# Optimization experiments

Hardware: AMD Instinct MI355X
Metric: run time of the kernel (lower is better)

## Reference

```python
import jax, jax.numpy as jnp
import numpy as np

B, IN, H = 4096, 1024, 1024

def setup_inputs() -> dict:
    key = jax.random.key(0)
    ks = jax.random.split(key, 8)
    s = 1.0 / np.sqrt(IN + H)  # ~torch Linear init scale
    return {
        "x": jax.random.normal(ks[0], (B, IN), jnp.float32),
        "h_prev": jax.random.normal(ks[1], (B, H), jnp.float32),
        "c_prev": jax.random.normal(ks[2], (B, H), jnp.float32),
        "Wf": jax.random.normal(ks[3], (IN + H, H), jnp.float32) * s,
        "bf": jnp.zeros((H,), jnp.float32),
        "Wi": jax.random.normal(ks[4], (IN + H, H), jnp.float32) * s,
        "bi": jnp.zeros((H,), jnp.float32),
        "Wg": jax.random.normal(ks[5], (IN + H, H), jnp.float32) * s,
        "bg": jnp.zeros((H,), jnp.float32),
        "Wo": jax.random.normal(ks[6], (IN + H, H), jnp.float32) * s,
        "bo": jnp.zeros((H,), jnp.float32),
    }

def reference(x, h_prev, c_prev, Wf, bf, Wi, bi, Wg, bg, Wo, bo):
    combined = jnp.concatenate([x, h_prev], axis=1)          # [B, IN+H]
    # fuse the 4 gate projections into one GEMM: [B, IN+H] x [IN+H, 4H]
    W = jnp.concatenate([Wf, Wi, Wg, Wo], axis=1)            # [IN+H, 4H]
    b = jnp.concatenate([bf, bi, bg, bo], axis=0)            # [4H]
    gates = combined @ W + b                                  # [B, 4H]
    f_t, i_t, g_t, o_t = jnp.split(gates, 4, axis=1)
    f_t = jax.nn.sigmoid(f_t)
    i_t = jax.nn.sigmoid(i_t)
    g_t = jnp.tanh(g_t)
    o_t = jax.nn.sigmoid(o_t)
    c_next = f_t * c_prev + i_t * g_t
    h_next = o_t * jnp.tanh(c_next)
    return (h_next, c_next)
```

## Files before the change

kernel.cpp:

```cpp
#include <hip/hip_runtime.h>

#define B_DIM 4096
#define H_DIM 1024
#define K_DIM 2048

typedef unsigned short u16;
typedef unsigned int u32;
typedef __attribute__((ext_vector_type(8))) short short8;
typedef __attribute__((ext_vector_type(4))) float f32x4;

typedef const __attribute__((address_space(1))) void* gas_ptr;
typedef __attribute__((address_space(3))) void* las_ptr;

#define WT_ELEMS (4 * H_DIM * K_DIM)
#define AC_ELEMS (B_DIM * K_DIM)
#define WS_NEEDED ((size_t)(WT_ELEMS + AC_ELEMS) * 2)

__device__ __forceinline__ void gl_lds16(const u16* g, u16* l) {
    __builtin_amdgcn_global_load_lds((gas_ptr)g, (las_ptr)l, 16, 0, 0);
}
__device__ __forceinline__ float bf2f(u16 v) {
    return __builtin_bit_cast(float, (u32)((u32)v << 16));
}
__device__ __forceinline__ u16 f2bf(float f) {
    u32 u = __builtin_bit_cast(u32, f);
    return (u16)((u + 0x7fffu + ((u >> 16) & 1u)) >> 16);
}
__device__ __forceinline__ float sigm(float x) { return 1.0f / (1.0f + __expf(-x)); }
__device__ __forceinline__ float tanh_f(float x) { return 1.0f - 2.0f / (__expf(2.0f * x) + 1.0f); }

__global__ __launch_bounds__(256) void prep_all(const float* __restrict__ x, const float* __restrict__ h,
                                                const float* __restrict__ Wf, const float* __restrict__ Wi,
                                                const float* __restrict__ Wg, const float* __restrict__ Wo,
                                                u16* __restrict__ A, u16* __restrict__ Wt) {
    const int t = threadIdx.x;
    if (blockIdx.x < 4096) {
        int e = (blockIdx.x * 256 + t) * 8;
        int m = e >> 11, c = e & 2047;
        const float* src = (c < 1024) ? (x + (size_t)m * 1024 + c) : (h + (size_t)m * 1024 + (c - 1024));
        float4 v0 = ((const float4*)src)[0], v1 = ((const float4*)src)[1];
        short8 q;
        q[0] = (short)f2bf(v0.x); q[1] = (short)f2bf(v0.y); q[2] = (short)f2bf(v0.z); q[3] = (short)f2bf(v0.w);
        q[4] = (short)f2bf(v1.x); q[5] = (short)f2bf(v1.y); q[6] = (short)f2bf(v1.z); q[7] = (short)f2bf(v1.w);
        *(short8*)(A + e) = q;
    } else {
        const int id = (blockIdx.x - 4096) * 4 + (t >> 6);
        const int l = t & 63;
        const int k0 = (id & 31) * 64, n0 = ((id >> 5) & 15) * 64, g = id >> 9;
        const float* W = (g == 0) ? Wf : (g == 1) ? Wi : (g == 2) ? Wg : Wo;
        const int no = (l & 7) * 8;
        const int ko = (l >> 3) * 8;
        float f[8][8];
#pragma unroll
        for (int j = 0; j < 8; ++j) {
            const float4* s = (const float4*)(W + (size_t)(k0 + ko + j) * H_DIM + n0 + no);
            float4 a = s[0], b = s[1];
            f[j][0] = a.x; f[j][1] = a.y; f[j][2] = a.z; f[j][3] = a.w;
            f[j][4] = b.x; f[j][5] = b.y; f[j][6] = b.z; f[j][7] = b.w;
        }
        u16* dst0 = Wt + (size_t)g * ((size_t)H_DIM * K_DIM) + (size_t)(n0 + no) * K_DIM + k0 + ko;
#pragma unroll
        for (int w2 = 0; w2 < 8; ++w2) {
            short8 q;
#pragma unroll
            for (int j = 0; j < 8; ++j) q[j] = (short)f2bf(f[j][w2]);
            *(short8*)(dst0 + (size_t)w2 * K_DIM) = q;
        }
    }
}

__global__ __launch_bounds__(256, 2) void lstm_gemm(
    const u16* __restrict__ A, const u16* __restrict__ Wt, const float* __restrict__ c_prev,
    const float* __restrict__ bf_, const float* __restrict__ bi_,
    const float* __restrict__ bg_, const float* __restrict__ bo_,
    float* __restrict__ out) {
    __shared__ u16 sA[256 * 64];
    __shared__ u16 sB[4 * 32 * 64];

    const int t = threadIdx.x;
    const int w = t >> 6;
    const int l = t & 63;
    const int quad = l >> 4;
    const int l15 = l & 15;
    const int v7 = l15 & 7;
    const int m0 = blockIdx.x * 256;
    const int j0 = blockIdx.y * 32;

    f32x4 acc[8][4];
#pragma unroll
    for (int nt = 0; nt < 8; ++nt)
#pragma unroll
        for (int mi = 0; mi < 4; ++mi)
            acc[nt][mi] = (f32x4){0.f, 0.f, 0.f, 0.f};

    const u16* pA[8];
    const u16* pB[4];
#pragma unroll
    for (int i = 0; i < 8; ++i) {
        int c = i * 256 + t;
        int m = c >> 3, slot = c & 7;
        pA[i] = A + (size_t)(m0 + m) * K_DIM + (slot ^ (m & 7)) * 8;
    }
#pragma unroll
    for (int i = 0; i < 4; ++i) {
        int c = i * 256 + t;
        int g = c >> 8, r = c & 255;
        int n = r >> 3, slot = r & 7;
        pB[i] = Wt + (size_t)g * (H_DIM * K_DIM) + (size_t)(j0 + n) * K_DIM + (slot ^ (n & 7)) * 8;
    }

    for (int kt = 0; kt < K_DIM / 64; ++kt) {
        __syncthreads();
#pragma unroll
        for (int i = 0; i < 8; ++i) {
            gl_lds16(pA[i], sA + (i * 256 + t) * 8);
            pA[i] += 64;
        }
#pragma unroll
        for (int i = 0; i < 4; ++i) {
            gl_lds16(pB[i], sB + (i * 256 + t) * 8);
            pB[i] += 64;
        }
        __syncthreads();

#pragma unroll
        for (int s = 0; s < 2; ++s) {
            const int sl = ((s * 4 + quad) ^ v7) * 8;
            short8 afr[4];
#pragma unroll
            for (int mi = 0; mi < 4; ++mi)
                afr[mi] = *(const short8*)(sA + (w * 64 + mi * 16 + l15) * 64 + sl);
            short8 bfr[8];
#pragma unroll
            for (int nt = 0; nt < 8; ++nt)
                bfr[nt] = *(const short8*)(sB + (nt >> 1) * 2048 + ((nt & 1) * 16 + l15) * 64 + sl);
#pragma unroll
            for (int nt = 0; nt < 8; ++nt)
#pragma unroll
                for (int mi = 0; mi < 4; ++mi)
                    acc[nt][mi] = __builtin_amdgcn_mfma_f32_16x16x32_bf16(afr[mi], bfr[nt], acc[nt][mi], 0, 0, 0);
        }
    }

#pragma unroll
    for (int ni = 0; ni < 2; ++ni) {
        const int col = j0 + ni * 16 + l15;
        const float bF = bf_[col], bI = bi_[col], bG = bg_[col], bO = bo_[col];
#pragma unroll
        for (int mi = 0; mi < 4; ++mi) {
            const int rowbase = m0 + w * 64 + mi * 16 + quad * 4;
            float cp[4];
#pragma unroll
            for (int rr = 0; rr < 4; ++rr)
                cp[rr] = c_prev[(size_t)(rowbase + rr) * H_DIM + col];
#pragma unroll
            for (int rr = 0; rr < 4; ++rr) {
                float fv = sigm(acc[0 + ni][mi][rr] + bF);
                float iv = sigm(acc[2 + ni][mi][rr] + bI);
                float gv = tanh_f(acc[4 + ni][mi][rr] + bG);
                float ov = sigm(acc[6 + ni][mi][rr] + bO);
                float cn = fv * cp[rr] + iv * gv;
                float hn = ov * tanh_f(cn);
                size_t idx = (size_t)(rowbase + rr) * H_DIM + col;
                out[idx] = hn;
                out[(size_t)B_DIM * H_DIM + idx] = cn;
            }
        }
    }
}

__global__ __launch_bounds__(256) void lstm_f32(
    const float* __restrict__ x, const float* __restrict__ h_prev, const float* __restrict__ c_prev,
    const float* __restrict__ Wf, const float* __restrict__ Wi, const float* __restrict__ Wg, const float* __restrict__ Wo,
    const float* __restrict__ bf_, const float* __restrict__ bi_, const float* __restrict__ bg_, const float* __restrict__ bo_,
    float* __restrict__ out) {
    __shared__ u16 smem[16384];
    u16* sA = smem;
    u16* sB = smem + 4096;

    const int t = threadIdx.x;
    const int w = t >> 6;
    const int l = t & 63;
    const int quad = l >> 4;
    const int l15 = l & 15;
    const int wr = w >> 1;
    const int wc = w & 1;
    const int m0 = blockIdx.x * 128;
    const int j0 = blockIdx.y * 32;

    const int arow = t >> 1;
    const int akh = (t & 1) * 16;
    const int r7 = t & 127;
    const int bk = r7 >> 2;
    const int bn8 = (r7 & 3) * 8;
    const int kswz = ((((bk >> 3) ^ (bn8 >> 3)) << 3) | (bk & 7));
    const float* WpA = (t < 128) ? Wf : Wi;
    const float* WpB = (t < 128) ? Wg : Wo;
    const int gA = (t >> 7);
    const int gB = 2 + (t >> 7);

    f32x4 acc[2][4][2];
#pragma unroll
    for (int gi = 0; gi < 2; ++gi)
#pragma unroll
        for (int mi = 0; mi < 4; ++mi)
#pragma unroll
            for (int ni = 0; ni < 2; ++ni)
                acc[gi][mi][ni] = (f32x4){0.f, 0.f, 0.f, 0.f};

    for (int kt = 0; kt < K_DIM / 32; ++kt) {
        const float* srcA = (kt < 32) ? x : h_prev;
        const int koff = (kt & 31) * 32;
        __syncthreads();

        const float4* ap = (const float4*)(srcA + (size_t)(m0 + arow) * H_DIM + koff + akh);
        float4 a0 = ap[0], a1 = ap[1], a2 = ap[2], a3 = ap[3];
        short8 p0, p1;
        p0[0] = (short)f2bf(a0.x); p0[1] = (short)f2bf(a0.y); p0[2] = (short)f2bf(a0.z); p0[3] = (short)f2bf(a0.w);
        p0[4] = (short)f2bf(a1.x); p0[5] = (short)f2bf(a1.y); p0[6] = (short)f2bf(a1.z); p0[7] = (short)f2bf(a1.w);
        p1[0] = (short)f2bf(a2.x); p1[1] = (short)f2bf(a2.y); p1[2] = (short)f2bf(a2.z); p1[3] = (short)f2bf(a2.w);
        p1[4] = (short)f2bf(a3.x); p1[5] = (short)f2bf(a3.y); p1[6] = (short)f2bf(a3.z); p1[7] = (short)f2bf(a3.w);
        *(short8*)(sA + arow * 32 + akh) = p0;
        *(short8*)(sA + arow * 32 + akh + 8) = p1;

        const float* gpA = WpA + (size_t)(kt * 32 + bk) * H_DIM + j0 + bn8;
        const float* gpB = WpB + (size_t)(kt * 32 + bk) * H_DIM + j0 + bn8;
        float4 c0 = *(const float4*)gpA, c1 = *(const float4*)(gpA + 4);
        float4 d0 = *(const float4*)gpB, d1 = *(const float4*)(gpB + 4);
        sB[gA * 1024 + (bn8 + 0) * 32 + kswz] = f2bf(c0.x);
        sB[gA * 1024 + (bn8 + 1) * 32 + kswz] = f2bf(c0.y);
        sB[gA * 1024 + (bn8 + 2) * 32 + kswz] = f2bf(c0.z);
        sB[gA * 1024 + (bn8 + 3) * 32 + kswz] = f2bf(c0.w);
        sB[gA * 1024 + (bn8 + 4) * 32 + kswz] = f2bf(c1.x);
        sB[gA * 1024 + (bn8 + 5) * 32 + kswz] = f2bf(c1.y);
        sB[gA * 1024 + (bn8 + 6) * 32 + kswz] = f2bf(c1.z);
        sB[gA * 1024 + (bn8 + 7) * 32 + kswz] = f2bf(c1.w);
        sB[gB * 1024 + (bn8 + 0) * 32 + kswz] = f2bf(d0.x);
        sB[gB * 1024 + (bn8 + 1) * 32 + kswz] = f2bf(d0.y);
        sB[gB * 1024 + (bn8 + 2) * 32 + kswz] = f2bf(d0.z);
        sB[gB * 1024 + (bn8 + 3) * 32 + kswz] = f2bf(d0.w);
        sB[gB * 1024 + (bn8 + 4) * 32 + kswz] = f2bf(d1.x);
        sB[gB * 1024 + (bn8 + 5) * 32 + kswz] = f2bf(d1.y);
        sB[gB * 1024 + (bn8 + 6) * 32 + kswz] = f2bf(d1.z);
        sB[gB * 1024 + (bn8 + 7) * 32 + kswz] = f2bf(d1.w);
        __syncthreads();

        short8 bfr[2][2];
#pragma unroll
        for (int gi = 0; gi < 2; ++gi) {
            int g = wc * 2 + gi;
#pragma unroll
            for (int ni = 0; ni < 2; ++ni) {
                int n = ni * 16 + l15;
                bfr[gi][ni] = *(const short8*)(sB + g * 1024 + n * 32 + ((quad ^ (n >> 3)) * 8));
            }
        }
#pragma unroll
        for (int mi = 0; mi < 4; ++mi) {
            int m = wr * 64 + mi * 16 + l15;
            short8 afr = *(const short8*)(sA + m * 32 + quad * 8);
#pragma unroll
            for (int gi = 0; gi < 2; ++gi)
#pragma unroll
                for (int ni = 0; ni < 2; ++ni)
                    acc[gi][mi][ni] =
                        __builtin_amdgcn_mfma_f32_16x16x32_bf16(afr, bfr[gi][ni], acc[gi][mi][ni], 0, 0, 0);
        }
    }

    __syncthreads();
#pragma unroll
    for (int gi = 0; gi < 2; ++gi) {
        int g = wc * 2 + gi;
        const float* bp = (g == 0) ? bf_ : (g == 1) ? bi_ : (g == 2) ? bg_ : bo_;
#pragma unroll
        for (int ni = 0; ni < 2; ++ni) {
            int col = ni * 16 + l15;
            float bias = bp[j0 + col];
#pragma unroll
            for (int mi = 0; mi < 4; ++mi)
#pragma unroll
                for (int rr = 0; rr < 4; ++rr) {
                    int row = wr * 64 + mi * 16 + quad * 4 + rr;
                    float v = acc[gi][mi][ni][rr] + bias;
                    v = (g == 2) ? tanh_f(v) : sigm(v);
                    smem[g * 4096 + row * 32 + col] = f2bf(v);
                }
        }
    }
    __syncthreads();

    const int col = t & 31;
    const int rb = t >> 5;
#pragma unroll
    for (int p = 0; p < 16; ++p) {
        int row = p * 8 + rb;
        float fv = bf2f(smem[0 * 4096 + row * 32 + col]);
        float iv = bf2f(smem[1 * 4096 + row * 32 + col]);
        float gv = bf2f(smem[2 * 4096 + row * 32 + col]);
        float ov = bf2f(smem[3 * 4096 + row * 32 + col]);
        size_t oidx = (size_t)(m0 + row) * H_DIM + j0 + col;
        float cp = c_prev[oidx];
        float cn = fv * cp + iv * gv;
        float hn = ov * tanh_f(cn);
        out[oidx] = hn;
        out[(size_t)B_DIM * H_DIM + oidx] = cn;
    }
}

extern "C" void kernel_launch(void* const* d_in, const int* in_sizes, int n_in,
                              void* d_out, int out_size, void* d_ws, size_t ws_size,
                              hipStream_t stream) {
    const float* x   = (const float*)d_in[0];
    const float* hp  = (const float*)d_in[1];
    const float* cp  = (const float*)d_in[2];
    const float* Wf  = (const float*)d_in[3];
    const float* bf_ = (const float*)d_in[4];
    const float* Wi  = (const float*)d_in[5];
    const float* bi_ = (const float*)d_in[6];
    const float* Wg  = (const float*)d_in[7];
    const float* bg_ = (const float*)d_in[8];
    const float* Wo  = (const float*)d_in[9];
    const float* bo_ = (const float*)d_in[10];

    if (ws_size >= WS_NEEDED) {
        u16* Wt = (u16*)d_ws;
        u16* Ac = (u16*)d_ws + WT_ELEMS;
        prep_all<<<dim3(4096 + 512), dim3(256), 0, stream>>>(x, hp, Wf, Wi, Wg, Wo, Ac, Wt);
        lstm_gemm<<<dim3(B_DIM / 256, H_DIM / 32), dim3(256), 0, stream>>>(
            Ac, Wt, cp, bf_, bi_, bg_, bo_, (float*)d_out);
    } else {
        lstm_f32<<<dim3(B_DIM / 128, H_DIM / 32), dim3(256), 0, stream>>>(
            x, hp, cp, Wf, Wi, Wg, Wo, bf_, bi_, bg_, bo_, (float*)d_out);
    }
}
```

Measured before the change: 211.5 us.

## Double-buffer GEMM tiles with 512-thread blocks and phased MFMA scheduling

Restructures the bf16 LSTM GEMM into 512-thread blocks that each cover a 256x(4x64) output tile, arranged as an 2x4 wave grid. LDS is double-buffered so the next K tile streams in via global_load_lds while MFMAs run on the current one. Explicit barriers, waitcnt, sched_barrier and setprio phases interleave the loads with MFMA groups. The aim is to hide global-load latency and raise arithmetic intensity per block. In exchange it uses 128KB of LDS per block, which may limit occupancy to one block per CU despite the launch bound, and relies on hand-tuned wait counts being correct.

```diff
diff --git a/kernel.cpp b/kernel.cpp
--- a/kernel.cpp
+++ b/kernel.cpp
@@ -3,6 +3,7 @@
 #define B_DIM 4096
 #define H_DIM 1024
 #define K_DIM 2048
+#define NTILE (K_DIM / 64)
 
 typedef unsigned short u16;
 typedef unsigned int u32;
@@ -69,13 +70,63 @@
     }
 }
 
-__global__ __launch_bounds__(256, 2) void lstm_gemm(
+#define PH_OPEN                                                  \
+    __builtin_amdgcn_s_barrier();                                \
+    asm volatile("s_waitcnt lgkmcnt(0)" ::: "memory");           \
+    __builtin_amdgcn_sched_barrier(0);                           \
+    __builtin_amdgcn_s_setprio(1)
+
+#define PH_CLOSE                                                 \
+    __builtin_amdgcn_s_setprio(0);                               \
+    __builtin_amdgcn_sched_barrier(0);                           \
+    __builtin_amdgcn_s_barrier();                                \
+    __builtin_amdgcn_sched_barrier(0)
+
+#define PH_CLOSE_VM2                                             \
+    __builtin_amdgcn_s_setprio(0);                               \
+    __builtin_amdgcn_sched_barrier(0);                           \
+    asm volatile("s_waitcnt vmcnt(2)" ::: "memory");             \
+    __builtin_amdgcn_s_barrier();                                \
+    __builtin_amdgcn_sched_barrier(0)
+
+#define PH_CLOSE_VM0                                             \
+    __builtin_amdgcn_s_setprio(0);                               \
+    __builtin_amdgcn_sched_barrier(0);                           \
+    asm volatile("s_waitcnt vmcnt(0)" ::: "memory");             \
+    __builtin_amdgcn_s_barrier();                                \
+    __builtin_amdgcn_sched_barrier(0)
+
+#define STG_A(NB, H)                                                              \
+    gl_lds16(pa[H][0], &sm[NB][(H) * 8192 + t * 8]);        pa[H][0] += 64;       \
+    gl_lds16(pa[H][1], &sm[NB][(H) * 8192 + 4096 + t * 8]); pa[H][1] += 64;
+
+#define STG_B(NB, H)                                                                      \
+    gl_lds16(pb[H][0], &sm[NB][16384 + (H) * 8192 + t * 8]);        pb[H][0] += 64;       \
+    gl_lds16(pb[H][1], &sm[NB][16384 + (H) * 8192 + 4096 + t * 8]); pb[H][1] += 64;
+
+#define RD_A(CB, KS)                                                                       \
+    _Pragma("unroll") for (int mi = 0; mi < 8; ++mi)                                       \
+        afr[mi] = *(const short8*)&sm[CB][(wr * 128 + mi * 16 + l15) * 64 +                \
+                                          ((((KS) * 4 + quad) ^ v7) * 8)];
+
+#define RD_B(CB, G, KS)                                                                    \
+    (*(const short8*)&sm[CB][16384 + (G) * 4096 + (wc * 16 + l15) * 64 +                   \
+                             ((((KS) * 4 + quad) ^ v7) * 8)])
+
+#define MFMA_PAIR(GP)                                                                      \
+    _Pragma("unroll") for (int mi = 0; mi < 8; ++mi)                                       \
+        acc[mi][2 * (GP)] = __builtin_amdgcn_mfma_f32_16x16x32_bf16(                       \
+            afr[mi], b0, acc[mi][2 * (GP)], 0, 0, 0);                                      \
+    _Pragma("unroll") for (int mi = 0; mi < 8; ++mi)                                       \
+        acc[mi][2 * (GP) + 1] = __builtin_amdgcn_mfma_f32_16x16x32_bf16(                   \
+            afr[mi], b1, acc[mi][2 * (GP) + 1], 0, 0, 0);
+
+__global__ __launch_bounds__(512, 2) void lstm_gemm(
     const u16* __restrict__ A, const u16* __restrict__ Wt, const float* __restrict__ c_prev,
     const float* __restrict__ bf_, const float* __restrict__ bi_,
     const float* __restrict__ bg_, const float* __restrict__ bo_,
     float* __restrict__ out) {
-    __shared__ u16 sA[256 * 64];
-    __shared__ u16 sB[4 * 32 * 64];
+    __shared__ u16 sm[2][32768];
 
     const int t = threadIdx.x;
     const int w = t >> 6;
@@ -83,88 +134,106 @@
     const int quad = l >> 4;
     const int l15 = l & 15;
     const int v7 = l15 & 7;
+    const int wr = w >> 2;
+    const int wc = w & 3;
     const int m0 = blockIdx.x * 256;
-    const int j0 = blockIdx.y * 32;
+    const int j0 = blockIdx.y * 64;
 
     f32x4 acc[8][4];
 #pragma unroll
-    for (int nt = 0; nt < 8; ++nt)
-#pragma unroll
-        for (int mi = 0; mi < 4; ++mi)
-            acc[nt][mi] = (f32x4){0.f, 0.f, 0.f, 0.f};
-
-    const u16* pA[8];
-    const u16* pB[4];
-#pragma unroll
-    for (int i = 0; i < 8; ++i) {
-        int c = i * 256 + t;
-        int m = c >> 3, slot = c & 7;
-        pA[i] = A + (size_t)(m0 + m) * K_DIM + (slot ^ (m & 7)) * 8;
-    }
-#pragma unroll
-    for (int i = 0; i < 4; ++i) {
-        int c = i * 256 + t;
-        int g = c >> 8, r = c & 255;
-        int n = r >> 3, slot = r & 7;
-        pB[i] = Wt + (size_t)g * (H_DIM * K_DIM) + (size_t)(j0 + n) * K_DIM + (slot ^ (n & 7)) * 8;
-    }
-
-    for (int kt = 0; kt < K_DIM / 64; ++kt) {
-        __syncthreads();
-#pragma unroll
-        for (int i = 0; i < 8; ++i) {
-            gl_lds16(pA[i], sA + (i * 256 + t) * 8);
-            pA[i] += 64;
-        }
-#pragma unroll
-        for (int i = 0; i < 4; ++i) {
-            gl_lds16(pB[i], sB + (i * 256 + t) * 8);
-            pB[i] += 64;
-        }
-        __syncthreads();
-
-#pragma unroll
-        for (int s = 0; s < 2; ++s) {
-            const int sl = ((s * 4 + quad) ^ v7) * 8;
-            short8 afr[4];
-#pragma unroll
-            for (int mi = 0; mi < 4; ++mi)
-                afr[mi] = *(const short8*)(sA + (w * 64 + mi * 16 + l15) * 64 + sl);
-            short8 bfr[8];
-#pragma unroll
-            for (int nt = 0; nt < 8; ++nt)
-                bfr[nt] = *(const short8*)(sB + (nt >> 1) * 2048 + ((nt & 1) * 16 + l15) * 64 + sl);
-#pragma unroll
-            for (int nt = 0; nt < 8; ++nt)
-#pragma unroll
-                for (int mi = 0; mi < 4; ++mi)
-                    acc[nt][mi] = __builtin_amdgcn_mfma_f32_16x16x32_bf16(afr[mi], bfr[nt], acc[nt][mi], 0, 0, 0);
-        }
-    }
-
-#pragma unroll
-    for (int ni = 0; ni < 2; ++ni) {
-        const int col = j0 + ni * 16 + l15;
-        const float bF = bf_[col], bI = bi_[col], bG = bg_[col], bO = bo_[col];
-#pragma unroll
-        for (int mi = 0; mi < 4; ++mi) {
-            const int rowbase = m0 + w * 64 + mi * 16 + quad * 4;
-            float cp[4];
-#pragma unroll
-            for (int rr = 0; rr < 4; ++rr)
-                cp[rr] = c_prev[(size_t)(rowbase + rr) * H_DIM + col];
-#pragma unroll
-            for (int rr = 0; rr < 4; ++rr) {
-                float fv = sigm(acc[0 + ni][mi][rr] + bF);
-                float iv = sigm(acc[2 + ni][mi][rr] + bI);
-                float gv = tanh_f(acc[4 + ni][mi][rr] + bG);
-                float ov = sigm(acc[6 + ni][mi][rr] + bO);
-                float cn = fv * cp[rr] + iv * gv;
-                float hn = ov * tanh_f(cn);
-                size_t idx = (size_t)(rowbase + rr) * H_DIM + col;
-                out[idx] = hn;
-                out[(size_t)B_DIM * H_DIM + idx] = cn;
-            }
+    for (int mi = 0; mi < 8; ++mi)
+#pragma unroll
+        for (int g = 0; g < 4; ++g)
+            acc[mi][g] = (f32x4){0.f, 0.f, 0.f, 0.f};
+
+    const u16* pa[2][2];
+    const u16* pb[2][2];
+#pragma unroll
+    for (int h = 0; h < 2; ++h)
+#pragma unroll
+        for (int i = 0; i < 2; ++i) {
+            int e = h * 8192 + (i * 512 + t) * 8;
+            int m = e >> 6, sl = (e >> 3) & 7;
+            pa[h][i] = A + (size_t)(m0 + m) * K_DIM + ((sl ^ (m & 7)) * 8);
+            int g = e >> 12, n = (e >> 6) & 63;
+            pb[h][i] = Wt + (size_t)g * ((size_t)H_DIM * K_DIM) + (size_t)(j0 + n) * K_DIM +
+                       ((sl ^ (n & 7)) * 8);
+        }
+
+    short8 afr[8], b0, b1;
+
+    STG_A(0, 0); STG_A(0, 1); STG_B(0, 0); STG_B(0, 1);
+    asm volatile("s_waitcnt vmcnt(2)" ::: "memory");
+    __builtin_amdgcn_s_barrier();
+    __builtin_amdgcn_sched_barrier(0);
+
+    for (int kt = 0; kt < NTILE - 1; ++kt) {
+        const int cb = kt & 1, nb = cb ^ 1;
+        RD_A(cb, 0);
+        b0 = RD_B(cb, 0, 0); b1 = RD_B(cb, 1, 0);
+        STG_A(nb, 0);
+        PH_OPEN;
+        MFMA_PAIR(0);
+        PH_CLOSE_VM2;
+        b0 = RD_B(cb, 2, 0); b1 = RD_B(cb, 3, 0);
+        STG_A(nb, 1);
+        PH_OPEN;
+        MFMA_PAIR(1);
+        PH_CLOSE;
+        RD_A(cb, 1);
+        b0 = RD_B(cb, 0, 1); b1 = RD_B(cb, 1, 1);
+        STG_B(nb, 0);
+        PH_OPEN;
+        MFMA_PAIR(0);
+        PH_CLOSE;
+        b0 = RD_B(cb, 2, 1); b1 = RD_B(cb, 3, 1);
+        STG_B(nb, 1);
+        PH_OPEN;
+        MFMA_PAIR(1);
+        PH_CLOSE_VM2;
+    }
+    {
+        const int cb = (NTILE - 1) & 1;
+        RD_A(cb, 0);
+        b0 = RD_B(cb, 0, 0); b1 = RD_B(cb, 1, 0);
+        PH_OPEN;
+        MFMA_PAIR(0);
+        PH_CLOSE_VM0;
+        b0 = RD_B(cb, 2, 0); b1 = RD_B(cb, 3, 0);
+        PH_OPEN;
+        MFMA_PAIR(1);
+        PH_CLOSE;
+        RD_A(cb, 1);
+        b0 = RD_B(cb, 0, 1); b1 = RD_B(cb, 1, 1);
+        PH_OPEN;
+        MFMA_PAIR(0);
+        PH_CLOSE;
+        b0 = RD_B(cb, 2, 1); b1 = RD_B(cb, 3, 1);
+        asm volatile("s_waitcnt lgkmcnt(0)" ::: "memory");
+        __builtin_amdgcn_sched_barrier(0);
+        MFMA_PAIR(1);
+    }
+
+    const int col = j0 + wc * 16 + l15;
+    const float bF = bf_[col], bI = bi_[col], bG = bg_[col], bO = bo_[col];
+#pragma unroll
+    for (int mi = 0; mi < 8; ++mi) {
+        const int rowbase = m0 + wr * 128 + mi * 16 + quad * 4;
+        float cp[4];
+#pragma unroll
+        for (int rr = 0; rr < 4; ++rr)
+            cp[rr] = c_prev[(size_t)(rowbase + rr) * H_DIM + col];
+#pragma unroll
+        for (int rr = 0; rr < 4; ++rr) {
+            float fv = sigm(acc[mi][0][rr] + bF);
+            float iv = sigm(acc[mi][1][rr] + bI);
+            float gv = tanh_f(acc[mi][2][rr] + bG);
+            float ov = sigm(acc[mi][3][rr] + bO);
+            float cn = fv * cp[rr] + iv * gv;
+            float hn = ov * tanh_f(cn);
+            size_t idx = (size_t)(rowbase + rr) * H_DIM + col;
+            out[idx] = hn;
+            out[(size_t)B_DIM * H_DIM + idx] = cn;
         }
     }
 }
@@ -327,7 +396,7 @@
         u16* Wt = (u16*)d_ws;
         u16* Ac = (u16*)d_ws + WT_ELEMS;
         prep_all<<<dim3(4096 + 512), dim3(256), 0, stream>>>(x, hp, Wf, Wi, Wg, Wo, Ac, Wt);
-        lstm_gemm<<<dim3(B_DIM / 256, H_DIM / 32), dim3(256), 0, stream>>>(
+        lstm_gemm<<<dim3(B_DIM / 256, H_DIM / 64), dim3(512), 0, stream>>>(
             Ac, Wt, cp, bf_, bi_, bg_, bo_, (float*)d_out);
     } else {
         lstm_f32<<<dim3(B_DIM / 128, H_DIM / 32), dim3(256), 0, stream>>>(
```

New measurement: 209.4 us. No clear change (-1.0%).

## Triple-buffer LDS in LSTM GEMM with 512-thread blocks and grid-strided prep

Applied to the files above, without the earlier changes.

Rewrites the bf16 GEMM main loop to use a three-stage LDS ring with K-tiles of 32, issuing the global-to-LDS loads for tile k+2 while tile k is computed. Only one barrier per iteration remains, paced by vmcnt waits instead of two full syncs. Blocks grow to 512 threads (8 waves in a 4x2 layout) with a smaller per-wave accumulator, and s_setprio is raised around the MFMA bursts. The prep kernel handles the activation cast with 512 blocks looping 8 times instead of 4096 one-shot blocks. The deeper pipeline is meant to hide memory latency, at the cost of more LDS per block and more complex wait-count bookkeeping.

```diff
diff --git a/kernel.cpp b/kernel.cpp
--- a/kernel.cpp
+++ b/kernel.cpp
@@ -3,6 +3,7 @@
 #define B_DIM 4096
 #define H_DIM 1024
 #define K_DIM 2048
+#define NT (K_DIM / 32)
 
 typedef unsigned short u16;
 typedef unsigned int u32;
@@ -34,17 +35,21 @@
                                                 const float* __restrict__ Wg, const float* __restrict__ Wo,
                                                 u16* __restrict__ A, u16* __restrict__ Wt) {
     const int t = threadIdx.x;
-    if (blockIdx.x < 4096) {
-        int e = (blockIdx.x * 256 + t) * 8;
-        int m = e >> 11, c = e & 2047;
-        const float* src = (c < 1024) ? (x + (size_t)m * 1024 + c) : (h + (size_t)m * 1024 + (c - 1024));
-        float4 v0 = ((const float4*)src)[0], v1 = ((const float4*)src)[1];
-        short8 q;
-        q[0] = (short)f2bf(v0.x); q[1] = (short)f2bf(v0.y); q[2] = (short)f2bf(v0.z); q[3] = (short)f2bf(v0.w);
-        q[4] = (short)f2bf(v1.x); q[5] = (short)f2bf(v1.y); q[6] = (short)f2bf(v1.z); q[7] = (short)f2bf(v1.w);
-        *(short8*)(A + e) = q;
+    if (blockIdx.x < 512) {
+#pragma unroll
+        for (int it = 0; it < 8; ++it) {
+            int e = it * (512 * 256 * 8) + (blockIdx.x * 256 + t) * 8;
+            int m = e >> 11, c = e & 2047;
+            const float* src = (c < 1024) ? (x + (size_t)m * 1024 + c)
+                                          : (h + (size_t)m * 1024 + (c - 1024));
+            float4 v0 = ((const float4*)src)[0], v1 = ((const float4*)src)[1];
+            short8 q;
+            q[0] = (short)f2bf(v0.x); q[1] = (short)f2bf(v0.y); q[2] = (short)f2bf(v0.z); q[3] = (short)f2bf(v0.w);
+            q[4] = (short)f2bf(v1.x); q[5] = (short)f2bf(v1.y); q[6] = (short)f2bf(v1.z); q[7] = (short)f2bf(v1.w);
+            *(short8*)(A + e) = q;
+        }
     } else {
-        const int id = (blockIdx.x - 4096) * 4 + (t >> 6);
+        const int id = (blockIdx.x - 512) * 4 + (t >> 6);
         const int l = t & 63;
         const int k0 = (id & 31) * 64, n0 = ((id >> 5) & 15) * 64, g = id >> 9;
         const float* W = (g == 0) ? Wf : (g == 1) ? Wi : (g == 2) ? Wg : Wo;
@@ -69,102 +74,116 @@
     }
 }
 
-__global__ __launch_bounds__(256, 2) void lstm_gemm(
+#define STG(C)                                                            \
+    gl_lds16(pa0, smu + (C) * 12288 + t * 8);        pa0 += 32;           \
+    gl_lds16(pa1, smu + (C) * 12288 + 4096 + t * 8); pa1 += 32;           \
+    gl_lds16(pb0, smu + (C) * 12288 + 8192 + t * 8); pb0 += 32;
+
+#define RD_A4(C)                                                          \
+    _Pragma("unroll") for (int mt = 0; mt < 4; ++mt)                      \
+        afr[mt] = *(const short8*)&smu[(C) * 12288 +                      \
+            (wr * 64 + mt * 16 + l15) * 32 + sl8];
+
+#define RD_BP(C, GP)                                                      \
+    _Pragma("unroll") for (int gi = 0; gi < 2; ++gi)                      \
+        bfr[gi] = *(const short8*)&smu[(C) * 12288 + 8192 +               \
+            (((GP) * 2 + gi) * 32 + wc * 16 + l15) * 32 + sl8];
+
+#define MFMA_H(GP)                                                        \
+    _Pragma("unroll") for (int mt = 0; mt < 4; ++mt)                      \
+    _Pragma("unroll") for (int gi = 0; gi < 2; ++gi)                      \
+        acc[mt][(GP) * 2 + gi] = __builtin_amdgcn_mfma_f32_16x16x32_bf16( \
+            afr[mt], bfr[gi], acc[mt][(GP) * 2 + gi], 0, 0, 0);
+
+__global__ __launch_bounds__(512, 4) void lstm_gemm(
     const u16* __restrict__ A, const u16* __restrict__ Wt, const float* __restrict__ c_prev,
     const float* __restrict__ bf_, const float* __restrict__ bi_,
     const float* __restrict__ bg_, const float* __restrict__ bo_,
     float* __restrict__ out) {
-    __shared__ u16 sA[256 * 64];
-    __shared__ u16 sB[4 * 32 * 64];
+    __shared__ u16 sm[3][12288];
+    u16* smu = &sm[0][0];
 
     const int t = threadIdx.x;
     const int w = t >> 6;
     const int l = t & 63;
     const int quad = l >> 4;
     const int l15 = l & 15;
-    const int v7 = l15 & 7;
+    const int kq = (l15 >> 2) & 3;
+    const int sl8 = ((quad ^ kq) & 3) * 8;
+    const int wr = w >> 1;
+    const int wc = w & 1;
     const int m0 = blockIdx.x * 256;
     const int j0 = blockIdx.y * 32;
 
-    f32x4 acc[8][4];
-#pragma unroll
-    for (int nt = 0; nt < 8; ++nt)
-#pragma unroll
-        for (int mi = 0; mi < 4; ++mi)
-            acc[nt][mi] = (f32x4){0.f, 0.f, 0.f, 0.f};
-
-    const u16* pA[8];
-    const u16* pB[4];
-#pragma unroll
-    for (int i = 0; i < 8; ++i) {
-        int c = i * 256 + t;
-        int m = c >> 3, slot = c & 7;
-        pA[i] = A + (size_t)(m0 + m) * K_DIM + (slot ^ (m & 7)) * 8;
-    }
-#pragma unroll
-    for (int i = 0; i < 4; ++i) {
-        int c = i * 256 + t;
-        int g = c >> 8, r = c & 255;
-        int n = r >> 3, slot = r & 7;
-        pB[i] = Wt + (size_t)g * (H_DIM * K_DIM) + (size_t)(j0 + n) * K_DIM + (slot ^ (n & 7)) * 8;
-    }
-
-    for (int kt = 0; kt < K_DIM / 64; ++kt) {
-        __syncthreads();
-#pragma unroll
-        for (int i = 0; i < 8; ++i) {
-            gl_lds16(pA[i], sA + (i * 256 + t) * 8);
-            pA[i] += 64;
-        }
-#pragma unroll
-        for (int i = 0; i < 4; ++i) {
-            gl_lds16(pB[i], sB + (i * 256 + t) * 8);
-            pB[i] += 64;
-        }
-        __syncthreads();
-
-#pragma unroll
-        for (int s = 0; s < 2; ++s) {
-            const int sl = ((s * 4 + quad) ^ v7) * 8;
-            short8 afr[4];
-#pragma unroll
-            for (int mi = 0; mi < 4; ++mi)
-                afr[mi] = *(const short8*)(sA + (w * 64 + mi * 16 + l15) * 64 + sl);
-            short8 bfr[8];
-#pragma unroll
-            for (int nt = 0; nt < 8; ++nt)
-                bfr[nt] = *(const short8*)(sB + (nt >> 1) * 2048 + ((nt & 1) * 16 + l15) * 64 + sl);
-#pragma unroll
-            for (int nt = 0; nt < 8; ++nt)
-#pragma unroll
-                for (int mi = 0; mi < 4; ++mi)
-                    acc[nt][mi] = __builtin_amdgcn_mfma_f32_16x16x32_bf16(afr[mi], bfr[nt], acc[nt][mi], 0, 0, 0);
-        }
-    }
-
-#pragma unroll
-    for (int ni = 0; ni < 2; ++ni) {
-        const int col = j0 + ni * 16 + l15;
-        const float bF = bf_[col], bI = bi_[col], bG = bg_[col], bO = bo_[col];
-#pragma unroll
-        for (int mi = 0; mi < 4; ++mi) {
-            const int rowbase = m0 + w * 64 + mi * 16 + quad * 4;
-            float cp[4];
-#pragma unroll
-            for (int rr = 0; rr < 4; ++rr)
-                cp[rr] = c_prev[(size_t)(rowbase + rr) * H_DIM + col];
-#pragma unroll
-            for (int rr = 0; rr < 4; ++rr) {
-                float fv = sigm(acc[0 + ni][mi][rr] + bF);
-                float iv = sigm(acc[2 + ni][mi][rr] + bI);
-                float gv = tanh_f(acc[4 + ni][mi][rr] + bG);
-                float ov = sigm(acc[6 + ni][mi][rr] + bO);
-                float cn = fv * cp[rr] + iv * gv;
-                float hn = ov * tanh_f(cn);
-                size_t idx = (size_t)(rowbase + rr) * H_DIM + col;
-                out[idx] = hn;
-                out[(size_t)B_DIM * H_DIM + idx] = cn;
-            }
+    f32x4 acc[4][4];
+#pragma unroll
+    for (int mt = 0; mt < 4; ++mt)
+#pragma unroll
+        for (int g = 0; g < 4; ++g)
+            acc[mt][g] = (f32x4){0.f, 0.f, 0.f, 0.f};
+
+    const int aphys = ((t & 3) ^ ((t >> 4) & 3)) * 8;
+    const u16* pa0 = A + (size_t)(m0 + (t >> 2)) * K_DIM + aphys;
+    const u16* pa1 = pa0 + (size_t)128 * K_DIM;
+    const u16* pb0 = Wt + (size_t)(t >> 7) * ((size_t)H_DIM * K_DIM) +
+                     (size_t)(j0 + ((t >> 2) & 31)) * K_DIM + aphys;
+
+    short8 afr[4], bfr[2];
+
+    STG(0); STG(1);
+    asm volatile("s_waitcnt vmcnt(3)" ::: "memory");
+    __builtin_amdgcn_s_barrier();
+
+    int c0 = 0, c1 = 1, c2 = 2;
+    for (int kt = 0; kt < NT - 2; ++kt) {
+        RD_A4(c0); RD_BP(c0, 0);
+        STG(c2);
+        __builtin_amdgcn_s_setprio(1);
+        MFMA_H(0);
+        RD_BP(c0, 1);
+        MFMA_H(1);
+        __builtin_amdgcn_s_setprio(0);
+        asm volatile("s_waitcnt vmcnt(3)" ::: "memory");
+        __builtin_amdgcn_s_barrier();
+        int tmp = c0; c0 = c1; c1 = c2; c2 = tmp;
+    }
+    {
+        RD_A4(c0); RD_BP(c0, 0);
+        __builtin_amdgcn_s_setprio(1);
+        MFMA_H(0);
+        RD_BP(c0, 1);
+        MFMA_H(1);
+        __builtin_amdgcn_s_setprio(0);
+        asm volatile("s_waitcnt vmcnt(0)" ::: "memory");
+        __builtin_amdgcn_s_barrier();
+    }
+    {
+        RD_A4(c1); RD_BP(c1, 0);
+        MFMA_H(0);
+        RD_BP(c1, 1);
+        MFMA_H(1);
+    }
+
+    const int col = j0 + wc * 16 + l15;
+    const float bF = bf_[col], bI = bi_[col], bG = bg_[col], bO = bo_[col];
+#pragma unroll
+    for (int mt = 0; mt < 4; ++mt) {
+        const int rowbase = m0 + wr * 64 + mt * 16 + quad * 4;
+        float cp[4];
+#pragma unroll
+        for (int rr = 0; rr < 4; ++rr)
+            cp[rr] = c_prev[(size_t)(rowbase + rr) * H_DIM + col];
+#pragma unroll
+        for (int rr = 0; rr < 4; ++rr) {
+            float fv = sigm(acc[mt][0][rr] + bF);
+            float iv = sigm(acc[mt][1][rr] + bI);
+            float gv = tanh_f(acc[mt][2][rr] + bG);
+            float ov = sigm(acc[mt][3][rr] + bO);
+            float cn = fv * cp[rr] + iv * gv;
+            float hn = ov * tanh_f(cn);
+            size_t idx = (size_t)(rowbase + rr) * H_DIM + col;
+            out[idx] = hn;
+            out[(size_t)B_DIM * H_DIM + idx] = cn;
         }
     }
 }
@@ -326,8 +345,8 @@
     if (ws_size >= WS_NEEDED) {
         u16* Wt = (u16*)d_ws;
         u16* Ac = (u16*)d_ws + WT_ELEMS;
-        prep_all<<<dim3(4096 + 512), dim3(256), 0, stream>>>(x, hp, Wf, Wi, Wg, Wo, Ac, Wt);
-        lstm_gemm<<<dim3(B_DIM / 256, H_DIM / 32), dim3(256), 0, stream>>>(
+        prep_all<<<dim3(1024), dim3(256), 0, stream>>>(x, hp, Wf, Wi, Wg, Wo, Ac, Wt);
+        lstm_gemm<<<dim3(B_DIM / 256, H_DIM / 32), dim3(512), 0, stream>>>(
             Ac, Wt, cp, bf_, bi_, bg_, bo_, (float*)d_out);
     } else {
         lstm_f32<<<dim3(B_DIM / 128, H_DIM / 32), dim3(256), 0, stream>>>(
```

Result: no change. 212.7 us (+0.6%).
